# Kernel tuning notes

Measured on AMD Instinct MI355X. Metric: run time of the kernel, lower is better.

The kernel has to match this reference:

```python
import jax, jax.numpy as jnp
import numpy as np

EPS = 1e-12  # matches torch F.normalize eps

def _l2norm(v, axis):
    n = jnp.linalg.norm(v, axis=axis, keepdims=True)
    return v / jnp.maximum(n, EPS)

def setup_inputs() -> dict:
    key = jax.random.key(0)
    k1, k2 = jax.random.split(key)
    x = jax.random.normal(k1, (16, 512, 64, 64), dtype=jnp.float32)
    mem = jax.random.normal(k2, (1024, 512), dtype=jnp.float32)
    memory = _l2norm(mem, axis=1)  # buffer initialized normalized, as in __init__
    return {"x": x, "memory": memory}

def reference(x, memory):
    B, C, H, W = x.shape
    feat = x.transpose(0, 2, 3, 1).reshape(-1, C)          # [N, C], N=B*H*W
    feat_norm = _l2norm(feat, axis=1)                       # [N, C]
    mem_norm = _l2norm(memory, axis=1)                      # [K, C]
    sim = feat_norm @ mem_norm.T                            # [N, K] cosine sims
    attn = jax.nn.softmax(sim, axis=1)                      # [N, K]
    recon = attn @ mem_norm                                 # [N, C]
    recon = recon.reshape(B, H, W, C).transpose(0, 3, 1, 2) # [B, C, H, W]
    match_map = attn.max(axis=1).reshape(B, H, W)           # [B, H, W]
    return recon, match_map
```

## Files before the change

### kernel.cpp

```cpp
#include <hip/hip_runtime.h>

#define C_DIM 512
#define K_MEM 1024

typedef __attribute__((ext_vector_type(8))) short short8;
typedef __attribute__((ext_vector_type(4))) float f32x4;
typedef __attribute__((ext_vector_type(16))) float f32x16;
typedef __attribute__((ext_vector_type(4))) unsigned int u32x4;

#define LGKM0()  asm volatile("s_waitcnt lgkmcnt(0)" ::: "memory")
#define VM0()    asm volatile("s_waitcnt vmcnt(0)" ::: "memory")
#define BAR()    { asm volatile("" ::: "memory"); __builtin_amdgcn_s_barrier(); asm volatile("" ::: "memory"); }

#define GLOAD16(dst, addr, imm) \
    asm volatile("global_load_dwordx4 %0, %1, off offset:%c2" \
                 : "=v"(dst) : "v"(addr), "n"(imm))
#define WAITV(N) do { asm volatile("s_waitcnt vmcnt(%c0)" :: "n"(N) : "memory"); \
                      __builtin_amdgcn_sched_barrier(0); } while (0)

__device__ __forceinline__ unsigned short f2bf(float f) {
    unsigned int u = __builtin_bit_cast(unsigned int, f);
    unsigned int r = (u + 0x7fffu + ((u >> 16) & 1u)) >> 16;
    return (unsigned short)r;
}

__device__ __forceinline__ f32x4 mfma16(short8 a, short8 b, f32x4 c) {
    return __builtin_amdgcn_mfma_f32_16x16x32_bf16(a, b, c, 0, 0, 0);
}
__device__ __forceinline__ f32x16 mfma32(short8 a, short8 b, f32x16 c) {
    return __builtin_amdgcn_mfma_f32_32x32x16_bf16(a, b, c, 0, 0, 0);
}

__device__ __forceinline__ void gl_lds16(const void* g, void* l) {
    __builtin_amdgcn_global_load_lds(
        (const __attribute__((address_space(1))) unsigned int*)g,
        (__attribute__((address_space(3))) unsigned int*)l, 16, 0, 0);
}

__global__ __launch_bounds__(256)
void prep_norm(const float* __restrict__ mem, unsigned short* __restrict__ Mn) {
    int k = blockIdx.x, t = threadIdx.x;
    const float* row = mem + (size_t)k * C_DIM;
    float2 v = *reinterpret_cast<const float2*>(row + 2 * t);
    float ss = v.x * v.x + v.y * v.y;
#pragma unroll
    for (int off = 32; off >= 1; off >>= 1) ss += __shfl_xor(ss, off);
    __shared__ float wp[4];
    if ((t & 63) == 0) wp[t >> 6] = ss;
    __syncthreads();
    float tot = wp[0] + wp[1] + wp[2] + wp[3];
    float rn = 1.0f / fmaxf(sqrtf(tot), 1e-12f);
    unsigned int pk = (unsigned int)f2bf(v.x * rn) | ((unsigned int)f2bf(v.y * rn) << 16);
    *reinterpret_cast<unsigned int*>(Mn + (size_t)k * C_DIM + 2 * t) = pk;
}

__global__ __launch_bounds__(256)
void prep_transpose(const unsigned short* __restrict__ Mn, unsigned short* __restrict__ MnT) {
    __shared__ unsigned short tl[64][72];
    int t = threadIdx.x;
    int bk = blockIdx.x & 15, bc = blockIdx.x >> 4;
    int k0 = bk * 64, c0 = bc * 64;
    {
        int kr = t >> 2, gc = (t & 3) * 16;
        const u32x4* src = reinterpret_cast<const u32x4*>(Mn + (size_t)(k0 + kr) * C_DIM + c0 + gc);
        u32x4 a = src[0], b = src[1];
        *reinterpret_cast<u32x4*>(&tl[kr][gc]) = a;
        *reinterpret_cast<u32x4*>(&tl[kr][gc + 8]) = b;
    }
    __syncthreads();
    {
        int cr = t >> 2, gk = (t & 3) * 16;
        unsigned int ow[8];
#pragma unroll
        for (int j = 0; j < 8; ++j)
            ow[j] = (unsigned int)tl[gk + 2 * j][cr] | ((unsigned int)tl[gk + 2 * j + 1][cr] << 16);
        unsigned int* dst = reinterpret_cast<unsigned int*>(MnT + (size_t)(c0 + cr) * K_MEM + k0 + gk);
#pragma unroll
        for (int j = 0; j < 8; ++j) dst[j] = ow[j];
    }
}

__global__ __launch_bounds__(512)
void normx_kernel(const float* __restrict__ x, unsigned short* __restrict__ Fn) {
    __shared__ alignas(16) char FnB[65536];
    __shared__ float normpart[64][9];
    __shared__ float rnormS[64];
    const int t = threadIdx.x, bid = blockIdx.x;
    const int b = bid >> 6, h = bid & 63;
    const int lane = t & 63, wv = t >> 6;
    const int w = lane, cg = wv;
    const float* xp = x + (size_t)b * 2097152 + (size_t)(cg * 64) * 4096 + (size_t)h * 64 + w;
    float xv[64];
#pragma unroll
    for (int i = 0; i < 64; ++i) xv[i] = xp[(size_t)i * 4096];
    float ss = 0.f;
#pragma unroll
    for (int i = 0; i < 64; ++i) ss += xv[i] * xv[i];
    normpart[w][cg] = ss;
    __syncthreads();
    if (t < 64) {
        float s = 0.f;
#pragma unroll
        for (int j = 0; j < 8; ++j) s += normpart[t][j];
        rnormS[t] = 1.0f / fmaxf(sqrtf(s), 1e-12f);
    }
    __syncthreads();
    float rn = rnormS[w];
    char* fnrow = FnB + w * 1024;
#pragma unroll
    for (int j = 0; j < 8; ++j) {
        u32x4 pk4;
#pragma unroll
        for (int p = 0; p < 4; ++p) {
            float v0 = xv[j * 8 + 2 * p] * rn;
            float v1 = xv[j * 8 + 2 * p + 1] * rn;
            pk4[p] = (unsigned int)f2bf(v0) | ((unsigned int)f2bf(v1) << 16);
        }
        int gs = (cg * 8 + j) ^ (w & 31);
        *(u32x4*)(fnrow + (gs << 4)) = pk4;
    }
    __syncthreads();
    const int r = t >> 3;
    char* orow = (char*)(Fn + (size_t)(bid * 64 + r) * C_DIM);
#pragma unroll
    for (int p = 0; p < 8; ++p) {
        int gl = p * 8 + (t & 7);
        u32x4 v = *(const u32x4*)(FnB + r * 1024 + ((gl ^ (r & 31)) << 4));
        *(u32x4*)(orow + gl * 16) = v;
    }
}

__device__ __forceinline__ void stage_tile(const char* g0, size_t rowBytes, int col0,
                                           char* lds0, int wv, int lane) {
#pragma unroll
    for (int j = 0; j < 4; ++j) {
        const int chunk = wv * 4 + j;
        const int r = chunk * 8 + (lane >> 3);
        const int gs = (lane & 7) ^ (r & 7);
        const char* src = g0 + (size_t)r * rowBytes + col0 + gs * 16;
        gl_lds16(src, lds0 + chunk * 1024);
    }
}

#define FRAG(base, r, gk) (*(const short8*)((base) + (r) * 128 + ((((gk)) ^ ((r) & 7)) << 4)))

__global__ __launch_bounds__(256, 4)
void gemm1_kernel(const unsigned short* __restrict__ Fn, const unsigned short* __restrict__ Mn,
                  unsigned short* __restrict__ P, float* __restrict__ Zp, float* __restrict__ Mp) {
    __shared__ alignas(16) char LDSU[34816];
    __shared__ float zS[128][2], zM[128][2];
    char* As = LDSU;
    char* Bs = LDSU + 16384;

    const int wg = (blockIdx.x & 7) * 512 + (blockIdx.x >> 3);
    const int mt = wg >> 3, nt = wg & 7;
    const int m0 = mt * 128, n0 = nt * 128;
    const int t = threadIdx.x, lane = t & 63, wv = t >> 6;
    const int wm = wv >> 1, wn = wv & 1;
    const int l15 = lane & 15, l4 = lane >> 4;

    const char* Ag = (const char*)Fn + (size_t)m0 * 1024;
    const char* Bg = (const char*)Mn + (size_t)n0 * 1024;

    f32x4 acc[4][4];
#pragma unroll
    for (int i = 0; i < 4; ++i)
#pragma unroll
        for (int j = 0; j < 4; ++j) acc[i][j] = (f32x4){0.f, 0.f, 0.f, 0.f};

#pragma unroll 1
    for (int kt = 0; kt < 8; ++kt) {
        stage_tile(Ag, 1024, kt * 128, As, wv, lane);
        stage_tile(Bg, 1024, kt * 128, Bs, wv, lane);
        VM0(); BAR();
#pragma unroll
        for (int ks = 0; ks < 2; ++ks) {
            short8 af[4], bfr[4];
#pragma unroll
            for (int i = 0; i < 4; ++i) {
                af[i]  = FRAG(As, wm * 64 + i * 16 + l15, ks * 4 + l4);
                bfr[i] = FRAG(Bs, wn * 64 + i * 16 + l15, ks * 4 + l4);
            }
#pragma unroll
            for (int mf = 0; mf < 4; ++mf)
#pragma unroll
                for (int nf = 0; nf < 4; ++nf)
                    acc[mf][nf] = mfma16(af[mf], bfr[nf], acc[mf][nf]);
        }
        LGKM0(); BAR();
    }

    float zsum[4][4], zmax[4][4];
#pragma unroll
    for (int mf = 0; mf < 4; ++mf)
#pragma unroll
        for (int r = 0; r < 4; ++r) { zsum[mf][r] = 0.f; zmax[mf][r] = 0.f; }
#pragma unroll
    for (int mf = 0; mf < 4; ++mf)
#pragma unroll
        for (int nf = 0; nf < 4; ++nf)
#pragma unroll
            for (int r = 0; r < 4; ++r) {
                float e = __expf(acc[mf][nf][r]);
                acc[mf][nf][r] = e;
                zsum[mf][r] += e;
                zmax[mf][r] = fmaxf(zmax[mf][r], e);
            }
#pragma unroll
    for (int off = 1; off < 16; off <<= 1)
#pragma unroll
        for (int mf = 0; mf < 4; ++mf)
#pragma unroll
            for (int r = 0; r < 4; ++r) {
                zsum[mf][r] += __shfl_xor(zsum[mf][r], off);
                zmax[mf][r] = fmaxf(zmax[mf][r], __shfl_xor(zmax[mf][r], off));
            }
    if (l15 == 0) {
#pragma unroll
        for (int mf = 0; mf < 4; ++mf)
#pragma unroll
            for (int r = 0; r < 4; ++r) {
                int row = wm * 64 + mf * 16 + l4 * 4 + r;
                zS[row][wn] = zsum[mf][r];
                zM[row][wn] = zmax[mf][r];
            }
    }
    char* Pscr = LDSU;
#pragma unroll
    for (int mf = 0; mf < 4; ++mf)
#pragma unroll
        for (int nf = 0; nf < 4; ++nf)
#pragma unroll
            for (int r = 0; r < 4; ++r) {
                int row = wm * 64 + mf * 16 + l4 * 4 + r;
                int col = wn * 64 + nf * 16 + l15;
                *(unsigned short*)(Pscr + row * 272 + col * 2) = f2bf(acc[mf][nf][r]);
            }
    LGKM0(); BAR();
    if (t < 128) {
        float zq = zS[t][0] + zS[t][1];
        float mq = fmaxf(zM[t][0], zM[t][1]);
        Zp[(size_t)(m0 + t) * 8 + nt] = zq;
        Mp[(size_t)(m0 + t) * 8 + nt] = mq;
    }
#pragma unroll
    for (int p = 0; p < 8; ++p) {
        int r = (t >> 4) + p * 16;
        u32x4 v = *(const u32x4*)(Pscr + r * 272 + (t & 15) * 16);
        *(u32x4*)((char*)P + (size_t)(m0 + r) * 2048 + n0 * 2 + (t & 15) * 16) = v;
    }
}

__global__ __launch_bounds__(256, 4)
void gemm2_kernel(const unsigned short* __restrict__ P, const unsigned short* __restrict__ MnT,
                  const float* __restrict__ Zp, const float* __restrict__ Mp,
                  float* __restrict__ recon, float* __restrict__ match) {
    __shared__ alignas(16) char As[16384];
    __shared__ alignas(16) char Bs[16384];
    __shared__ float zinvS[128];

    const int wg = (blockIdx.x & 7) * 256 + (blockIdx.x >> 3);
    const int mt = wg >> 2, nt = wg & 3;
    const int m0 = mt * 128, n0 = nt * 128;
    const int t = threadIdx.x, lane = t & 63, wv = t >> 6;
    const int wm = wv >> 1, wn = wv & 1;
    const int l15 = lane & 15, l4 = lane >> 4;

    if (t < 128) {
        f32x4 a = *(const f32x4*)(Zp + (size_t)(m0 + t) * 8);
        f32x4 b = *(const f32x4*)(Zp + (size_t)(m0 + t) * 8 + 4);
        float s = (a[0] + a[1] + a[2] + a[3]) + (b[0] + b[1] + b[2] + b[3]);
        float zi = 1.0f / s;
        zinvS[t] = zi;
        if (nt == 0) {
            f32x4 c = *(const f32x4*)(Mp + (size_t)(m0 + t) * 8);
            f32x4 d = *(const f32x4*)(Mp + (size_t)(m0 + t) * 8 + 4);
            float m = fmaxf(fmaxf(fmaxf(c[0], c[1]), fmaxf(c[2], c[3])),
                            fmaxf(fmaxf(d[0], d[1]), fmaxf(d[2], d[3])));
            match[m0 + t] = m * zi;
        }
    }

    const char* Ag = (const char*)P + (size_t)m0 * 2048;
    const char* Bg = (const char*)MnT + (size_t)n0 * 2048;

    f32x4 acc[4][4];
#pragma unroll
    for (int i = 0; i < 4; ++i)
#pragma unroll
        for (int j = 0; j < 4; ++j) acc[i][j] = (f32x4){0.f, 0.f, 0.f, 0.f};

#pragma unroll 1
    for (int kt = 0; kt < 16; ++kt) {
        stage_tile(Ag, 2048, kt * 128, As, wv, lane);
        stage_tile(Bg, 2048, kt * 128, Bs, wv, lane);
        VM0(); BAR();
#pragma unroll
        for (int ks = 0; ks < 2; ++ks) {
            short8 af[4], bfr[4];
#pragma unroll
            for (int i = 0; i < 4; ++i) {
                af[i]  = FRAG(As, wm * 64 + i * 16 + l15, ks * 4 + l4);
                bfr[i] = FRAG(Bs, wn * 64 + i * 16 + l15, ks * 4 + l4);
            }
#pragma unroll
            for (int mf = 0; mf < 4; ++mf)
#pragma unroll
                for (int nf = 0; nf < 4; ++nf)
                    acc[mf][nf] = mfma16(af[mf], bfr[nf], acc[mf][nf]);
        }
        LGKM0(); BAR();
    }

    const int b = m0 >> 12;
    const int inb0 = m0 & 4095;
#pragma unroll
    for (int mf = 0; mf < 4; ++mf) {
        f32x4 zv = *(const f32x4*)(&zinvS[wm * 64 + mf * 16 + l4 * 4]);
#pragma unroll
        for (int nf = 0; nf < 4; ++nf) {
            f32x4 v = acc[mf][nf];
            v[0] *= zv[0]; v[1] *= zv[1]; v[2] *= zv[2]; v[3] *= zv[3];
            int c = n0 + wn * 64 + nf * 16 + l15;
            int inb = inb0 + wm * 64 + mf * 16 + l4 * 4;
            *(f32x4*)(recon + (size_t)b * 2097152 + (size_t)c * 4096 + inb) = v;
        }
    }
}

__global__ __launch_bounds__(512)
__attribute__((amdgpu_waves_per_eu(2, 2)))
void fused_attn(const float* __restrict__ x,
                const unsigned short* __restrict__ Mn,
                const unsigned short* __restrict__ MnT,
                float* __restrict__ recon,
                float* __restrict__ match) {
    __shared__ alignas(16) char FnB[65536];
    __shared__ alignas(16) char PldsB[2 * 32768];
    __shared__ float Zinv[64], rnormS[64];

    const int t = threadIdx.x;
    const int bid = blockIdx.x;
    const int b = bid >> 6, h = bid & 63;
    const int lane = t & 63, wv = t >> 6;
    const int l31 = lane & 31, l5 = lane >> 5;
    const int ko = wv;
    const int cb = wv * 64;

    {
        float* normpart = (float*)PldsB;
        const int w = lane, cg = wv;
        const float* xp = x + (size_t)b * 2097152 + (size_t)(cg * 64) * 4096 + (size_t)h * 64 + w;
        float xv[64];
#pragma unroll
        for (int i = 0; i < 64; ++i) xv[i] = xp[(size_t)i * 4096];
        float ss = 0.f;
#pragma unroll
        for (int i = 0; i < 64; ++i) ss += xv[i] * xv[i];
        normpart[w * 9 + cg] = ss;
        __syncthreads();
        if (t < 64) {
            float s = 0.f;
#pragma unroll
            for (int j = 0; j < 8; ++j) s += normpart[t * 9 + j];
            rnormS[t] = 1.0f / fmaxf(sqrtf(s), 1e-12f);
        }
        __syncthreads();
        float rn = rnormS[w];
        char* fnrow = FnB + w * 1024;
#pragma unroll
        for (int j = 0; j < 8; ++j) {
            u32x4 pk4;
#pragma unroll
            for (int p = 0; p < 4; ++p) {
                float v0 = xv[j * 8 + 2 * p] * rn;
                float v1 = xv[j * 8 + 2 * p + 1] * rn;
                pk4[p] = (unsigned int)f2bf(v0) | ((unsigned int)f2bf(v1) << 16);
            }
            int gs = (cg * 8 + j) ^ (w & 31);
            *(u32x4*)(fnrow + (gs << 4)) = pk4;
        }
    }
    __syncthreads();

    f32x16 acc3[2][2];
#pragma unroll
    for (int i = 0; i < 2; ++i)
#pragma unroll
        for (int j = 0; j < 2; ++j)
#pragma unroll
            for (int r = 0; r < 16; ++r) acc3[i][j][r] = 0.f;

    float regZ[2] = {0.f, 0.f};
    float regM[2] = {-3.0e38f, -3.0e38f};
    const char* fnR0 = FnB + l31 * 1024;
    const char* fnR1 = FnB + (32 + l31) * 1024;

#pragma unroll 1
    for (int kt = 0; kt < 4; ++kt) {
        const char* aG = (const char*)Mn + ((size_t)(kt * 256 + ko * 32 + l31) << 10) + (l5 << 4);
        u32x4 afb[2][4];
        GLOAD16(afb[0][0], aG, 0);
        GLOAD16(afb[0][1], aG, 32);
        GLOAD16(afb[0][2], aG, 64);
        GLOAD16(afb[0][3], aG, 96);
        f32x16 acc1[2];
#pragma unroll
        for (int j = 0; j < 2; ++j)
#pragma unroll
            for (int r = 0; r < 16; ++r) acc1[j][r] = 0.f;
#pragma unroll
        for (int g = 0; g < 8; ++g) {
            if (g < 7) {
#pragma unroll
                for (int s = 0; s < 4; ++s)
                    GLOAD16(afb[(g + 1) & 1][s], aG, ((g + 1) * 4 + s) * 32);
                WAITV(4);
            } else {
                WAITV(0);
            }
#pragma unroll
            for (int s = 0; s < 4; ++s) {
                const int st = g * 4 + s;
                const int gsw = (((st << 1) | l5) ^ l31) << 4;
                short8 b0 = *(const short8*)(fnR0 + gsw);
                short8 b1 = *(const short8*)(fnR1 + gsw);
                short8 av = __builtin_bit_cast(short8, afb[g & 1][s]);
                acc1[0] = mfma32(av, b0, acc1[0]);
                acc1[1] = mfma32(av, b1, acc1[1]);
            }
        }
        const char* aG2a = (const char*)MnT + ((size_t)(cb + l31) << 11) + ((size_t)kt << 9) + (l5 << 4);
        const char* aG2b = aG2a + 65536;
        u32x4 a2b[2][4];
        GLOAD16(a2b[0][0], aG2a, 0);
        GLOAD16(a2b[0][1], aG2b, 0);
        GLOAD16(a2b[0][2], aG2a, 32);
        GLOAD16(a2b[0][3], aG2b, 32);
        unsigned int P32[2][8];
#pragma unroll
        for (int nt = 0; nt < 2; ++nt) {
            float s0 = 0.f, m0 = -3.0e38f;
#pragma unroll
            for (int j = 0; j < 8; ++j) {
                float a0 = acc1[nt][2 * j], a1 = acc1[nt][2 * j + 1];
                m0 = fmaxf(m0, fmaxf(a0, a1));
                float e0 = __expf(a0), e1 = __expf(a1);
                P32[nt][j] = (unsigned int)f2bf(e0) | ((unsigned int)f2bf(e1) << 16);
                s0 += e0 + e1;
            }
            s0 += __shfl_xor(s0, 32);
            m0 = fmaxf(m0, __shfl_xor(m0, 32));
            regZ[nt] += s0;
            regM[nt] = fmaxf(regM[nt], m0);
        }
        char* Pb = PldsB + (kt & 1) * 32768;
#pragma unroll
        for (int nt = 0; nt < 2; ++nt) {
            const int n = nt * 32 + l31;
            char* prow = Pb + n * 512;
#pragma unroll
            for (int jp = 0; jp < 4; ++jp) {
                const int gk = ko * 4 + jp;
                uint2 v;
                v.x = P32[nt][2 * jp];
                v.y = P32[nt][2 * jp + 1];
                *(uint2*)(prow + ((gk ^ (n & 31)) << 4) + 8 * l5) = v;
            }
        }
        LGKM0(); BAR();
#pragma unroll
        for (int g = 0; g < 8; ++g) {
            if (g < 7) {
#pragma unroll
                for (int u = 0; u < 2; ++u) {
                    GLOAD16(a2b[(g + 1) & 1][u * 2 + 0], aG2a, ((g + 1) * 2 + u) * 32);
                    GLOAD16(a2b[(g + 1) & 1][u * 2 + 1], aG2b, ((g + 1) * 2 + u) * 32);
                }
                WAITV(4);
            } else {
                WAITV(0);
            }
#pragma unroll
            for (int u = 0; u < 2; ++u) {
                const int ks = g * 2 + u;
                const int gsw = (((ks << 1) | l5) ^ l31) << 4;
                short8 bp0 = *(const short8*)(Pb + l31 * 512 + gsw);
                short8 bp1 = *(const short8*)(Pb + (32 + l31) * 512 + gsw);
                short8 a0 = __builtin_bit_cast(short8, a2b[g & 1][u * 2 + 0]);
                short8 a1 = __builtin_bit_cast(short8, a2b[g & 1][u * 2 + 1]);
                acc3[0][0] = mfma32(a0, bp0, acc3[0][0]);
                acc3[0][1] = mfma32(a0, bp1, acc3[0][1]);
                acc3[1][0] = mfma32(a1, bp0, acc3[1][0]);
                acc3[1][1] = mfma32(a1, bp1, acc3[1][1]);
            }
        }
    }
    {
        float* pS = (float*)FnB;
        float* pM = (float*)(FnB + 2048);
        if (l5 == 0) {
            pS[ko * 64 + l31] = regZ[0];
            pS[ko * 64 + 32 + l31] = regZ[1];
            pM[ko * 64 + l31] = regM[0];
            pM[ko * 64 + 32 + l31] = regM[1];
        }
        LGKM0(); BAR();
        if (t < 64) {
            float s = 0.f, m = -3.0e38f;
#pragma unroll
            for (int k8 = 0; k8 < 8; ++k8) {
                s += pS[k8 * 64 + t];
                m = fmaxf(m, pM[k8 * 64 + t]);
            }
            float zi = 1.0f / s;
            Zinv[t] = zi;
            match[(size_t)bid * 64 + t] = __expf(m) * zi;
        }
        LGKM0(); BAR();
    }
    const float zi0 = Zinv[l31], zi1 = Zinv[32 + l31];
    float* rbase = recon + (size_t)b * 2097152 + (size_t)h * 64;
#pragma unroll
    for (int ct = 0; ct < 2; ++ct) {
#pragma unroll
        for (int r = 0; r < 16; ++r) {
            const int c = cb + ct * 32 + (r & 3) + 8 * (r >> 2) + 4 * l5;
            float* rp = rbase + (size_t)c * 4096;
            rp[l31] = acc3[ct][0][r] * zi0;
            rp[32 + l31] = acc3[ct][1][r] * zi1;
        }
    }
}

extern "C" void kernel_launch(void* const* d_in, const int* in_sizes, int n_in,
                              void* d_out, int out_size, void* d_ws, size_t ws_size,
                              hipStream_t stream) {
    (void)in_sizes; (void)n_in; (void)out_size;
    if (ws_size < (size_t)2 * 1024 * 1024) return;

    const float* x = (const float*)d_in[0];
    const float* mem = (const float*)d_in[1];
    float* recon = (float*)d_out;
    float* match = recon + (size_t)16 * 512 * 64 * 64;
    char* ws = (char*)d_ws;
    unsigned short* Mn = (unsigned short*)ws;
    unsigned short* MnT = (unsigned short*)(ws + 1048576);

    prep_norm<<<dim3(K_MEM), dim3(256), 0, stream>>>(mem, Mn);
    prep_transpose<<<dim3(128), dim3(256), 0, stream>>>(Mn, MnT);

    const size_t NEED = 207618048ull;
    if (ws_size >= NEED) {
        unsigned short* Fn = (unsigned short*)(ws + 2097152);
        unsigned short* P  = (unsigned short*)(ws + 69206016);
        float* Zp = (float*)(ws + 203423744);
        float* Mp = (float*)(ws + 205520896);
        normx_kernel<<<dim3(1024), dim3(512), 0, stream>>>(x, Fn);
        gemm1_kernel<<<dim3(4096), dim3(256), 0, stream>>>(Fn, Mn, P, Zp, Mp);
        gemm2_kernel<<<dim3(2048), dim3(256), 0, stream>>>(P, MnT, Zp, Mp, recon, match);
    } else {
        fused_attn<<<dim3(1024), dim3(512), 0, stream>>>(x, Mn, MnT, recon, match);
    }
}
```

Before: 266.9 us.

## Double-buffer LDS tiles in both GEMM K-loops to overlap loads with MFMA

Measured after the change: 279.9 us. 4.9% more time.

```diff
diff --git a/kernel.cpp b/kernel.cpp
--- a/kernel.cpp
+++ b/kernel.cpp
@@ -144,13 +144,42 @@
 
 #define FRAG(base, r, gk) (*(const short8*)((base) + (r) * 128 + ((((gk)) ^ ((r) & 7)) << 4)))
 
-__global__ __launch_bounds__(256, 4)
+#define GEMM_KLOOP_DBUF(NKT, ABYT, BBYT)                                                 \
+    stage_tile(Ag, ABYT, 0, LDSU, wv, lane);                                             \
+    stage_tile(Bg, BBYT, 0, LDSU + 16384, wv, lane);                                     \
+    VM0(); BAR();                                                                        \
+    _Pragma("unroll 1")                                                                  \
+    for (int kt = 0; kt < (NKT); ++kt) {                                                 \
+        char* As = LDSU + (kt & 1) * 32768;                                              \
+        char* Bs = As + 16384;                                                           \
+        if (kt + 1 < (NKT)) {                                                            \
+            char* nb = LDSU + ((kt + 1) & 1) * 32768;                                    \
+            stage_tile(Ag, ABYT, (kt + 1) * 128, nb, wv, lane);                          \
+            stage_tile(Bg, BBYT, (kt + 1) * 128, nb + 16384, wv, lane);                  \
+        }                                                                                \
+        _Pragma("unroll")                                                                \
+        for (int ks = 0; ks < 2; ++ks) {                                                 \
+            short8 af[4], bfr[4];                                                        \
+            _Pragma("unroll")                                                            \
+            for (int i = 0; i < 4; ++i) {                                                \
+                af[i]  = FRAG(As, wm * 64 + i * 16 + l15, ks * 4 + l4);                  \
+                bfr[i] = FRAG(Bs, wn * 64 + i * 16 + l15, ks * 4 + l4);                  \
+            }                                                                            \
+            _Pragma("unroll")                                                            \
+            for (int mf = 0; mf < 4; ++mf)                                               \
+                _Pragma("unroll")                                                        \
+                for (int nf = 0; nf < 4; ++nf)                                           \
+                    acc[mf][nf] = mfma16(af[mf], bfr[nf], acc[mf][nf]);                  \
+        }                                                                                \
+        if (kt + 1 < (NKT)) { VM0(); }                                                   \
+        BAR();                                                                           \
+    }
+
+__global__ __launch_bounds__(256)
 void gemm1_kernel(const unsigned short* __restrict__ Fn, const unsigned short* __restrict__ Mn,
                   unsigned short* __restrict__ P, float* __restrict__ Zp, float* __restrict__ Mp) {
-    __shared__ alignas(16) char LDSU[34816];
+    __shared__ alignas(16) char LDSU[65536];
     __shared__ float zS[128][2], zM[128][2];
-    char* As = LDSU;
-    char* Bs = LDSU + 16384;
 
     const int wg = (blockIdx.x & 7) * 512 + (blockIdx.x >> 3);
     const int mt = wg >> 3, nt = wg & 7;
@@ -168,27 +197,7 @@
 #pragma unroll
         for (int j = 0; j < 4; ++j) acc[i][j] = (f32x4){0.f, 0.f, 0.f, 0.f};
 
-#pragma unroll 1
-    for (int kt = 0; kt < 8; ++kt) {
-        stage_tile(Ag, 1024, kt * 128, As, wv, lane);
-        stage_tile(Bg, 1024, kt * 128, Bs, wv, lane);
-        VM0(); BAR();
-#pragma unroll
-        for (int ks = 0; ks < 2; ++ks) {
-            short8 af[4], bfr[4];
-#pragma unroll
-            for (int i = 0; i < 4; ++i) {
-                af[i]  = FRAG(As, wm * 64 + i * 16 + l15, ks * 4 + l4);
-                bfr[i] = FRAG(Bs, wn * 64 + i * 16 + l15, ks * 4 + l4);
-            }
-#pragma unroll
-            for (int mf = 0; mf < 4; ++mf)
-#pragma unroll
-                for (int nf = 0; nf < 4; ++nf)
-                    acc[mf][nf] = mfma16(af[mf], bfr[nf], acc[mf][nf]);
-        }
-        LGKM0(); BAR();
-    }
+    GEMM_KLOOP_DBUF(8, 1024, 1024)
 
     float zsum[4][4], zmax[4][4];
 #pragma unroll
@@ -251,12 +260,11 @@
     }
 }
 
-__global__ __launch_bounds__(256, 4)
+__global__ __launch_bounds__(256)
 void gemm2_kernel(const unsigned short* __restrict__ P, const unsigned short* __restrict__ MnT,
                   const float* __restrict__ Zp, const float* __restrict__ Mp,
                   float* __restrict__ recon, float* __restrict__ match) {
-    __shared__ alignas(16) char As[16384];
-    __shared__ alignas(16) char Bs[16384];
+    __shared__ alignas(16) char LDSU[65536];
     __shared__ float zinvS[128];
 
     const int wg = (blockIdx.x & 7) * 256 + (blockIdx.x >> 3);
@@ -290,27 +298,7 @@
 #pragma unroll
         for (int j = 0; j < 4; ++j) acc[i][j] = (f32x4){0.f, 0.f, 0.f, 0.f};
 
-#pragma unroll 1
-    for (int kt = 0; kt < 16; ++kt) {
-        stage_tile(Ag, 2048, kt * 128, As, wv, lane);
-        stage_tile(Bg, 2048, kt * 128, Bs, wv, lane);
-        VM0(); BAR();
-#pragma unroll
-        for (int ks = 0; ks < 2; ++ks) {
-            short8 af[4], bfr[4];
-#pragma unroll
-            for (int i = 0; i < 4; ++i) {
-                af[i]  = FRAG(As, wm * 64 + i * 16 + l15, ks * 4 + l4);
-                bfr[i] = FRAG(Bs, wn * 64 + i * 16 + l15, ks * 4 + l4);
-            }
-#pragma unroll
-            for (int mf = 0; mf < 4; ++mf)
-#pragma unroll
-                for (int nf = 0; nf < 4; ++nf)
-                    acc[mf][nf] = mfma16(af[mf], bfr[nf], acc[mf][nf]);
-        }
-        LGKM0(); BAR();
-    }
+    GEMM_KLOOP_DBUF(16, 2048, 2048)
 
     const int b = m0 >> 12;
     const int inb0 = m0 & 4095;
```
